# Optimization experiments

Hardware: AMD Instinct MI355X
Metric: run time of the kernel (lower is better)

## Reference

```python
import jax, jax.numpy as jnp
import numpy as np
import math

N_HEADS = 16

def setup_inputs() -> dict:
    key = jax.random.key(0)
    ks = jax.random.split(key, 5)
    B, S, D = 4, 2048, 1024
    scale = 0.02
    return {
        "x": jax.random.normal(ks[0], (B, S, D), dtype=jnp.float32),
        "w_in": jax.random.normal(ks[1], (D, 3 * D), dtype=jnp.float32) * scale,
        "b_in": jax.random.normal(ks[2], (3 * D,), dtype=jnp.float32) * scale,
        "w_out": jax.random.normal(ks[3], (D, D), dtype=jnp.float32) * scale,
        "b_out": jax.random.normal(ks[4], (D,), dtype=jnp.float32) * scale,
    }

def reference(x, w_in, b_in, w_out, b_out):
    B, S, D = x.shape
    H = N_HEADS
    dh = D // H
    qkv = x @ w_in + b_in                      # [B,S,3D]
    q, k, v = jnp.split(qkv, 3, axis=-1)
    # [B,S,D] -> [B,H,S,dh]
    q = q.reshape(B, S, H, dh).transpose(0, 2, 1, 3)
    k = k.reshape(B, S, H, dh).transpose(0, 2, 1, 3)
    v = v.reshape(B, S, H, dh).transpose(0, 2, 1, 3)
    scores = jnp.einsum("bhqd,bhkd->bhqk", q, k) / math.sqrt(dh)
    causal = jnp.tril(jnp.ones((S, S), dtype=bool))  # allow k <= q
    scores = jnp.where(causal, scores, -jnp.inf)
    wei = jax.nn.softmax(scores, axis=-1)
    out = jnp.einsum("bhqk,bhkd->bhqd", wei, v)      # [B,H,S,dh]
    out = out.transpose(0, 2, 1, 3).reshape(B, S, D)
    return out @ w_out + b_out
```

## Files before the change

kernel.cpp:

```cpp
#include <hip/hip_runtime.h>

typedef unsigned short u16;
typedef unsigned int   u32;
typedef float  f32x4  __attribute__((ext_vector_type(4)));
typedef __bf16 bf16x8 __attribute__((ext_vector_type(8)));
typedef __bf16 bf16x4 __attribute__((ext_vector_type(4)));
typedef short  s16x4  __attribute__((ext_vector_type(4)));
typedef unsigned short u16x8 __attribute__((ext_vector_type(8)));
typedef unsigned int   u32x4 __attribute__((ext_vector_type(4)));

__device__ __forceinline__ u16 f2bf(float f) {
  u32 u = __builtin_bit_cast(u32, f);
  u = (u + 0x7fffu + ((u >> 16) & 1u)) >> 16;
  return (u16)u;
}

__device__ __forceinline__ void gload_lds16(const void* g, void* l) {
  __builtin_amdgcn_global_load_lds(
      (const __attribute__((address_space(1))) void*)g,
      (__attribute__((address_space(3))) void*)l, 16, 0, 0);
}

__global__ __launch_bounds__(256) void conv_f32_bf16(
    const float* __restrict__ in, u16* __restrict__ out, int n8) {
  int i = blockIdx.x * 256 + threadIdx.x;
  if (i >= n8) return;
  const float4* p = (const float4*)in;
  float4 a = p[2 * i], b = p[2 * i + 1];
  u16x8 r;
  r[0] = f2bf(a.x); r[1] = f2bf(a.y); r[2] = f2bf(a.z); r[3] = f2bf(a.w);
  r[4] = f2bf(b.x); r[5] = f2bf(b.y); r[6] = f2bf(b.z); r[7] = f2bf(b.w);
  ((u16x8*)out)[i] = r;
}

__global__ __launch_bounds__(256) void conv_transpose(
    const float* __restrict__ in, u16* __restrict__ out, int K, int N) {
  __shared__ float tile[64][65];
  int nb = N >> 6;
  int tk = blockIdx.x / nb, tn = blockIdx.x % nb;
  int t = threadIdx.x;
  int kl = t >> 4, n4 = (t & 15) * 4;
#pragma unroll
  for (int i = 0; i < 4; ++i) {
    int k = kl + 16 * i;
    float4 v = *(const float4*)(in + (size_t)(tk * 64 + k) * N + tn * 64 + n4);
    tile[k][n4] = v.x; tile[k][n4 + 1] = v.y; tile[k][n4 + 2] = v.z; tile[k][n4 + 3] = v.w;
  }
  __syncthreads();
  int nl = t >> 4, k4 = (t & 15) * 4;
#pragma unroll
  for (int i = 0; i < 4; ++i) {
    int n = nl + 16 * i;
    ushort4 o;
    o.x = f2bf(tile[k4 + 0][n]); o.y = f2bf(tile[k4 + 1][n]);
    o.z = f2bf(tile[k4 + 2][n]); o.w = f2bf(tile[k4 + 3][n]);
    *(ushort4*)(out + (size_t)(tn * 64 + n) * K + tk * 64 + k4) = o;
  }
}

template <int OUT_BF16>
__global__ __launch_bounds__(256, 2) void gemm_kernel(
    const u16* __restrict__ A, const u16* __restrict__ Bt,
    const float* __restrict__ bias, void* __restrict__ C,
    int M, int N, int K) {
  __shared__ __align__(16) char smem[32768];
  char* As = smem;
  char* Bs = smem + 16384;
  int tid = threadIdx.x, w = tid >> 6, lane = tid & 63;
  int g = lane >> 4, l15 = lane & 15, l7 = lane & 7;
  int nblk = N >> 7;
  int bm = blockIdx.x / nblk, bn = blockIdx.x % nblk;
  int m0 = bm << 7, n0 = bn << 7;
  int wm = w >> 1, wn = w & 1;

  f32x4 acc[4][4];
#pragma unroll
  for (int i = 0; i < 4; ++i)
#pragma unroll
    for (int j = 0; j < 4; ++j) acc[i][j] = f32x4{0.f, 0.f, 0.f, 0.f};

  int kiter = K >> 6;
  for (int kt = 0; kt < kiter; ++kt) {
    __syncthreads();
#pragma unroll
    for (int i = 0; i < 4; ++i) {
      int rbase = 32 * w + 8 * i;
      int row = rbase + (lane >> 3);
      int koff = kt * 64 + 8 * (l7 ^ (row & 7));
      gload_lds16(A + (size_t)(m0 + row) * K + koff, As + rbase * 128);
      gload_lds16(Bt + (size_t)(n0 + row) * K + koff, Bs + rbase * 128);
    }
    __syncthreads();
#pragma unroll
    for (int ks = 0; ks < 2; ++ks) {
      bf16x8 af[4], bf[4];
#pragma unroll
      for (int mi = 0; mi < 4; ++mi) {
        int ml = wm * 64 + mi * 16 + l15;
        af[mi] = *(const bf16x8*)(As + ml * 128 + ((ks * 64 + g * 16) ^ ((ml & 7) << 4)));
      }
#pragma unroll
      for (int ni = 0; ni < 4; ++ni) {
        int nl = wn * 64 + ni * 16 + l15;
        bf[ni] = *(const bf16x8*)(Bs + nl * 128 + ((ks * 64 + g * 16) ^ ((nl & 7) << 4)));
      }
#pragma unroll
      for (int mi = 0; mi < 4; ++mi)
#pragma unroll
        for (int ni = 0; ni < 4; ++ni)
          acc[mi][ni] = __builtin_amdgcn_mfma_f32_16x16x32_bf16(af[mi], bf[ni], acc[mi][ni], 0, 0, 0);
    }
  }

#pragma unroll
  for (int ni = 0; ni < 4; ++ni) {
    int col = n0 + wn * 64 + ni * 16 + l15;
    float bv = bias[col];
#pragma unroll
    for (int mi = 0; mi < 4; ++mi) {
      int rowb = m0 + wm * 64 + mi * 16 + g * 4;
#pragma unroll
      for (int r = 0; r < 4; ++r) {
        float v = acc[mi][ni][r] + bv;
        if (OUT_BF16)
          ((u16*)C)[(size_t)(rowb + r) * N + col] = f2bf(v);
        else
          ((float*)C)[(size_t)(rowb + r) * N + col] = v;
      }
    }
  }
}


#if __has_builtin(__builtin_amdgcn_mfma_f32_16x16x16bf16_1k)
#define HAVE_MFMA16 1
__device__ __forceinline__ f32x4 mfma16(s16x4 a, s16x4 b, f32x4 c) {
  return __builtin_amdgcn_mfma_f32_16x16x16bf16_1k(a, b, c, 0, 0, 0);
}
#endif

struct V2reg { u16x8 a, b; };

__device__ __forceinline__ void stage_k(const u16* qb, char* kbuf, int kvt,
                                        int h, int w, int lane) {
  int l7 = lane & 7;
#pragma unroll
  for (int i = 0; i < 2; ++i) {
    int rbase = w * 16 + i * 8;
    int row = rbase + (lane >> 3);
    const u16* src = qb + (size_t)(kvt * 64 + row) * 3072 + 1024 + h * 64 + 8 * (l7 ^ (row & 7));
    gload_lds16(src, kbuf + rbase * 128);
  }
}

__device__ __forceinline__ V2reg load_v(const u16* qb, int kvt, int h, int kv0, int d0) {
  const u16* vs = qb + (size_t)(kvt * 64 + kv0) * 3072 + 2048 + h * 64 + d0;
  V2reg r;
  r.a = *(const u16x8*)vs;
  r.b = *(const u16x8*)(vs + 3072);
  return r;
}

__device__ __forceinline__ void write_v(char* vbuf, V2reg v, int kv0, int d0) {
#pragma unroll
  for (int j = 0; j < 8; ++j) {
    int d = d0 + j;
    u32 val = (u32)v.a[j] | ((u32)v.b[j] << 16);
    int sw = ((d & 7) ^ (d >> 3)) << 4;
    *(u32*)(vbuf + d * 128 + ((2 * kv0) ^ sw)) = val;
  }
}

__global__ __launch_bounds__(256, 2) void attn_fwd(
    const u16* __restrict__ qkv, u16* __restrict__ aout) {
  const int S = 2048, D3 = 3072;
  int bh = blockIdx.x & 63;
  int qt = 31 - (blockIdx.x >> 6);
  int b = bh >> 4, h = bh & 15;
  const u16* qb = qkv + (size_t)b * S * D3;

  int tid = threadIdx.x;
  int w = tid >> 6, lane = tid & 63;
  int g = lane >> 4, l15 = lane & 15, l7 = lane & 7;

  __shared__ __align__(16) char Kb[2][8192];
  __shared__ __align__(16) char Vb[2][8192];

  int qrow = qt * 64 + w * 16 + l15;
  const u16* qp = qb + (size_t)qrow * D3 + h * 64 + g * 8;
  bf16x8 qf0 = *(const bf16x8*)qp;
  bf16x8 qf1 = *(const bf16x8*)(qp + 32);

  f32x4 oaT[4];
#pragma unroll
  for (int i = 0; i < 4; ++i) oaT[i] = f32x4{0.f, 0.f, 0.f, 0.f};
  float m_s = -3e38f, l_s = 0.f;

  int vkv0 = w * 16 + ((lane >> 3) << 1);
  int vd0 = l7 * 8;

  stage_k(qb, Kb[0], 0, h, w, lane);
  {
    V2reg v = load_v(qb, 0, h, vkv0, vd0);
    write_v(Vb[0], v, vkv0, vd0);
  }
  __syncthreads();

  V2reg vreg;
  for (int kvt = 0; kvt <= qt; ++kvt) {
    int cur = kvt & 1;
    if (kvt < qt) {
      stage_k(qb, Kb[cur ^ 1], kvt + 1, h, w, lane);
      vreg = load_v(qb, kvt + 1, h, vkv0, vd0);
    }

    f32x4 sT[4];
    __builtin_amdgcn_s_setprio(1);
#pragma unroll
    for (int nb = 0; nb < 4; ++nb) {
      int kv = nb * 16 + l15;
      const char* kb = Kb[cur] + kv * 128;
      int sw = (kv & 7) << 4;
      bf16x8 kf0 = *(const bf16x8*)(kb + ((g * 16) ^ sw));
      bf16x8 kf1 = *(const bf16x8*)(kb + ((64 + g * 16) ^ sw));
      f32x4 z = {0.f, 0.f, 0.f, 0.f};
      z = __builtin_amdgcn_mfma_f32_16x16x32_bf16(kf0, qf0, z, 0, 0, 0);
      z = __builtin_amdgcn_mfma_f32_16x16x32_bf16(kf1, qf1, z, 0, 0, 0);
      sT[nb] = z;
    }
    __builtin_amdgcn_s_setprio(0);

#pragma unroll
    for (int nb = 0; nb < 4; ++nb)
#pragma unroll
      for (int r = 0; r < 4; ++r) sT[nb][r] *= 0.125f;
    if (kvt == qt) {
      int qloc = w * 16 + l15;
#pragma unroll
      for (int nb = 0; nb < 4; ++nb)
#pragma unroll
        for (int r = 0; r < 4; ++r)
          if (nb * 16 + g * 4 + r > qloc) sT[nb][r] = -1e30f;
    }

    float pm = -3e38f;
#pragma unroll
    for (int nb = 0; nb < 4; ++nb)
#pragma unroll
      for (int r = 0; r < 4; ++r) pm = fmaxf(pm, sT[nb][r]);
    pm = fmaxf(pm, __shfl_xor(pm, 16));
    pm = fmaxf(pm, __shfl_xor(pm, 32));
    float newm = fmaxf(m_s, pm);
    float corr = __expf(m_s - newm);
    float rs = 0.f;
#pragma unroll
    for (int nb = 0; nb < 4; ++nb)
#pragma unroll
      for (int r = 0; r < 4; ++r) {
        float e = __expf(sT[nb][r] - newm);
        sT[nb][r] = e;
        rs += e;
      }
    rs += __shfl_xor(rs, 16);
    rs += __shfl_xor(rs, 32);
    l_s = l_s * corr + rs;
    m_s = newm;
#pragma unroll
    for (int db = 0; db < 4; ++db)
#pragma unroll
      for (int r = 0; r < 4; ++r) oaT[db][r] *= corr;

#ifdef HAVE_MFMA16
    s16x4 pf[4];
#pragma unroll
    for (int nb = 0; nb < 4; ++nb) {
      bf16x4 t;
#pragma unroll
      for (int r = 0; r < 4; ++r) t[r] = (__bf16)sT[nb][r];
      pf[nb] = __builtin_bit_cast(s16x4, t);
    }
    __builtin_amdgcn_s_setprio(1);
#pragma unroll
    for (int db = 0; db < 4; ++db) {
      int d = db * 16 + l15;
      const char* vb = Vb[cur] + d * 128;
      int swd = ((d & 7) ^ (d >> 3)) << 4;
#pragma unroll
      for (int nb = 0; nb < 4; ++nb) {
        bf16x4 vf = *(const bf16x4*)(vb + ((nb * 32 + g * 8) ^ swd));
        oaT[db] = mfma16(__builtin_bit_cast(s16x4, vf), pf[nb], oaT[db]);
      }
    }
    __builtin_amdgcn_s_setprio(0);
#else
    u32 wlo[4], whi[4];
#pragma unroll
    for (int nb = 0; nb < 4; ++nb) {
      wlo[nb] = (u32)f2bf(sT[nb][0]) | ((u32)f2bf(sT[nb][1]) << 16);
      whi[nb] = (u32)f2bf(sT[nb][2]) | ((u32)f2bf(sT[nb][3]) << 16);
    }
    int srcA = (2 * (g & 1)) * 16 + l15;
    int srcB = srcA + 16;
    bool hi = (g >> 1) != 0;
    __builtin_amdgcn_s_setprio(1);
#pragma unroll
    for (int kb2 = 0; kb2 < 2; ++kb2) {
      int nbE = kb2 * 2, nbO = kb2 * 2 + 1;
      u32 a0 = __shfl(wlo[nbE], srcA), a1 = __shfl(whi[nbE], srcA);
      u32 a2 = __shfl(wlo[nbE], srcB), a3 = __shfl(whi[nbE], srcB);
      u32 b0 = __shfl(wlo[nbO], srcA), b1 = __shfl(whi[nbO], srcA);
      u32 b2 = __shfl(wlo[nbO], srcB), b3 = __shfl(whi[nbO], srcB);
      u32x4 ow = {hi ? b0 : a0, hi ? b1 : a1, hi ? b2 : a2, hi ? b3 : a3};
      bf16x8 pfrag = __builtin_bit_cast(bf16x8, ow);
#pragma unroll
      for (int db = 0; db < 4; ++db) {
        int d = db * 16 + l15;
        int swd = ((d & 7) ^ (d >> 3)) << 4;
        bf16x8 vf = *(const bf16x8*)(Vb[cur] + d * 128 + ((kb2 * 64 + g * 16) ^ swd));
        oaT[db] = __builtin_amdgcn_mfma_f32_16x16x32_bf16(vf, pfrag, oaT[db], 0, 0, 0);
      }
    }
    __builtin_amdgcn_s_setprio(0);
#endif

    if (kvt < qt) {
      write_v(Vb[cur ^ 1], vreg, vkv0, vd0);
      __syncthreads();
    }
  }

  float inv = 1.0f / l_s;
  size_t obase = (size_t)(b * S + qt * 64 + w * 16 + l15) * 1024 + h * 64;
#pragma unroll
  for (int db = 0; db < 4; ++db) {
    ushort4 st;
    st.x = f2bf(oaT[db][0] * inv);
    st.y = f2bf(oaT[db][1] * inv);
    st.z = f2bf(oaT[db][2] * inv);
    st.w = f2bf(oaT[db][3] * inv);
    *(ushort4*)(aout + obase + db * 16 + g * 4) = st;
  }
}

extern "C" void kernel_launch(void* const* d_in, const int* in_sizes, int n_in,
                              void* d_out, int out_size, void* d_ws, size_t ws_size,
                              hipStream_t stream) {
  (void)in_sizes; (void)n_in; (void)out_size;
  const float* x     = (const float*)d_in[0];
  const float* w_in  = (const float*)d_in[1];
  const float* b_in  = (const float*)d_in[2];
  const float* w_out = (const float*)d_in[3];
  const float* b_out = (const float*)d_in[4];
  float* out = (float*)d_out;
  char* ws = (char*)d_ws;
  if (ws_size < 92274688u) return;

  u16* xb     = (u16*)(ws);
  u16* w_inT  = (u16*)(ws + (16u << 20));
  u16* w_outT = (u16*)(ws + (22u << 20));
  u16* qkv    = (u16*)(ws + (24u << 20));
  u16* aout   = (u16*)(ws + (72u << 20));

  conv_f32_bf16<<<4096, 256, 0, stream>>>(x, xb, 1048576);
  conv_transpose<<<768, 256, 0, stream>>>(w_in, w_inT, 1024, 3072);
  conv_transpose<<<256, 256, 0, stream>>>(w_out, w_outT, 1024, 1024);
  gemm_kernel<1><<<1536, 256, 0, stream>>>(xb, w_inT, b_in, qkv, 8192, 3072, 1024);
  attn_fwd<<<2048, 256, 0, stream>>>(qkv, aout);
  gemm_kernel<0><<<512, 256, 0, stream>>>(aout, w_outT, b_out, out, 8192, 1024, 1024);
}
```

Baseline: 261.9 us.

## Fold softmax scale into QKV GEMM, lazy rescale, MFMA row sums, XCD block remap

The QKV GEMM epilogue now multiplies Q columns by 0.125*log2(e), so attention can drop its per-score scaling and use exp2 directly. The online softmax rescales the running max only when some lane's max grows by more than 8, which skips most correction multiplies. Row sums are accumulated by an MFMA against a vector of ones instead of shuffle reductions. The GEMMs also remap block ids across the 8 XCDs, and the attention launch bound is raised to 4 blocks per CU. Costs are an extra MFMA per tile, an extra bf16 rounding of the scaled Q values, a small overflow margin from the lazy max, and tighter register limits that could cause spills.

```diff
diff --git a/kernel.cpp b/kernel.cpp
--- a/kernel.cpp
+++ b/kernel.cpp
@@ -58,7 +58,7 @@
   }
 }
 
-template <int OUT_BF16>
+template <int OUT_BF16, int SCALE_Q>
 __global__ __launch_bounds__(256, 2) void gemm_kernel(
     const u16* __restrict__ A, const u16* __restrict__ Bt,
     const float* __restrict__ bias, void* __restrict__ C,
@@ -68,8 +68,10 @@
   char* Bs = smem + 16384;
   int tid = threadIdx.x, w = tid >> 6, lane = tid & 63;
   int g = lane >> 4, l15 = lane & 15, l7 = lane & 7;
+  int cpx = (int)gridDim.x >> 3;
+  int bid = (blockIdx.x & 7) * cpx + (blockIdx.x >> 3);
   int nblk = N >> 7;
-  int bm = blockIdx.x / nblk, bn = blockIdx.x % nblk;
+  int bm = bid / nblk, bn = bid % nblk;
   int m0 = bm << 7, n0 = bn << 7;
   int wm = w >> 1, wn = w & 1;
 
@@ -116,12 +118,13 @@
   for (int ni = 0; ni < 4; ++ni) {
     int col = n0 + wn * 64 + ni * 16 + l15;
     float bv = bias[col];
+    float sc = (SCALE_Q && col < 1024) ? 0.18033688011112042f : 1.0f;
 #pragma unroll
     for (int mi = 0; mi < 4; ++mi) {
       int rowb = m0 + wm * 64 + mi * 16 + g * 4;
 #pragma unroll
       for (int r = 0; r < 4; ++r) {
-        float v = acc[mi][ni][r] + bv;
+        float v = (acc[mi][ni][r] + bv) * sc;
         if (OUT_BF16)
           ((u16*)C)[(size_t)(rowb + r) * N + col] = f2bf(v);
         else
@@ -171,7 +174,7 @@
   }
 }
 
-__global__ __launch_bounds__(256, 2) void attn_fwd(
+__global__ __launch_bounds__(256, 4) void attn_fwd(
     const u16* __restrict__ qkv, u16* __restrict__ aout) {
   const int S = 2048, D3 = 3072;
   int bh = blockIdx.x & 63;
@@ -194,7 +197,8 @@
   f32x4 oaT[4];
 #pragma unroll
   for (int i = 0; i < 4; ++i) oaT[i] = f32x4{0.f, 0.f, 0.f, 0.f};
-  float m_s = -3e38f, l_s = 0.f;
+  f32x4 l_acc = {0.f, 0.f, 0.f, 0.f};
+  float m_s = -3e38f;
 
   int vkv0 = w * 16 + ((lane >> 3) << 1);
   int vd0 = l7 * 8;
@@ -230,10 +234,6 @@
     }
     __builtin_amdgcn_s_setprio(0);
 
-#pragma unroll
-    for (int nb = 0; nb < 4; ++nb)
-#pragma unroll
-      for (int r = 0; r < 4; ++r) sT[nb][r] *= 0.125f;
     if (kvt == qt) {
       int qloc = w * 16 + l15;
 #pragma unroll
@@ -250,25 +250,21 @@
       for (int r = 0; r < 4; ++r) pm = fmaxf(pm, sT[nb][r]);
     pm = fmaxf(pm, __shfl_xor(pm, 16));
     pm = fmaxf(pm, __shfl_xor(pm, 32));
-    float newm = fmaxf(m_s, pm);
-    float corr = __expf(m_s - newm);
-    float rs = 0.f;
+    if (!__all(pm - m_s <= 8.0f)) {
+      float newm = fmaxf(m_s, pm);
+      float corr = __builtin_amdgcn_exp2f(m_s - newm);
+      m_s = newm;
+      l_acc[0] *= corr;
+#pragma unroll
+      for (int db = 0; db < 4; ++db)
+#pragma unroll
+        for (int r = 0; r < 4; ++r) oaT[db][r] *= corr;
+    }
 #pragma unroll
     for (int nb = 0; nb < 4; ++nb)
 #pragma unroll
-      for (int r = 0; r < 4; ++r) {
-        float e = __expf(sT[nb][r] - newm);
-        sT[nb][r] = e;
-        rs += e;
-      }
-    rs += __shfl_xor(rs, 16);
-    rs += __shfl_xor(rs, 32);
-    l_s = l_s * corr + rs;
-    m_s = newm;
-#pragma unroll
-    for (int db = 0; db < 4; ++db)
-#pragma unroll
-      for (int r = 0; r < 4; ++r) oaT[db][r] *= corr;
+      for (int r = 0; r < 4; ++r)
+        sT[nb][r] = __builtin_amdgcn_exp2f(sT[nb][r] - m_s);
 
 #ifdef HAVE_MFMA16
     s16x4 pf[4];
@@ -279,7 +275,12 @@
       for (int r = 0; r < 4; ++r) t[r] = (__bf16)sT[nb][r];
       pf[nb] = __builtin_bit_cast(s16x4, t);
     }
+    s16x4 ones;
+#pragma unroll
+    for (int r = 0; r < 4; ++r) ones[r] = (short)0x3F80;
     __builtin_amdgcn_s_setprio(1);
+#pragma unroll
+    for (int nb = 0; nb < 4; ++nb) l_acc = mfma16(ones, pf[nb], l_acc);
 #pragma unroll
     for (int db = 0; db < 4; ++db) {
       int d = db * 16 + l15;
@@ -302,6 +303,9 @@
     int srcA = (2 * (g & 1)) * 16 + l15;
     int srcB = srcA + 16;
     bool hi = (g >> 1) != 0;
+    bf16x8 ones8;
+#pragma unroll
+    for (int j = 0; j < 8; ++j) ones8[j] = __builtin_bit_cast(__bf16, (u16)0x3F80);
     __builtin_amdgcn_s_setprio(1);
 #pragma unroll
     for (int kb2 = 0; kb2 < 2; ++kb2) {
@@ -312,6 +316,7 @@
       u32 b2 = __shfl(wlo[nbO], srcB), b3 = __shfl(whi[nbO], srcB);
       u32x4 ow = {hi ? b0 : a0, hi ? b1 : a1, hi ? b2 : a2, hi ? b3 : a3};
       bf16x8 pfrag = __builtin_bit_cast(bf16x8, ow);
+      l_acc = __builtin_amdgcn_mfma_f32_16x16x32_bf16(ones8, pfrag, l_acc, 0, 0, 0);
 #pragma unroll
       for (int db = 0; db < 4; ++db) {
         int d = db * 16 + l15;
@@ -329,7 +334,7 @@
     }
   }
 
-  float inv = 1.0f / l_s;
+  float inv = 1.0f / l_acc[0];
   size_t obase = (size_t)(b * S + qt * 64 + w * 16 + l15) * 1024 + h * 64;
 #pragma unroll
   for (int db = 0; db < 4; ++db) {
@@ -364,7 +369,7 @@
   conv_f32_bf16<<<4096, 256, 0, stream>>>(x, xb, 1048576);
   conv_transpose<<<768, 256, 0, stream>>>(w_in, w_inT, 1024, 3072);
   conv_transpose<<<256, 256, 0, stream>>>(w_out, w_outT, 1024, 1024);
-  gemm_kernel<1><<<1536, 256, 0, stream>>>(xb, w_inT, b_in, qkv, 8192, 3072, 1024);
+  gemm_kernel<1, 1><<<1536, 256, 0, stream>>>(xb, w_inT, b_in, qkv, 8192, 3072, 1024);
   attn_fwd<<<2048, 256, 0, stream>>>(qkv, aout);
-  gemm_kernel<0><<<512, 256, 0, stream>>>(aout, w_outT, b_out, out, 8192, 1024, 1024);
-}
+  gemm_kernel<0, 0><<<512, 256, 0, stream>>>(aout, w_outT, b_out, out, 8192, 1024, 1024);
+}
```

Result: no change. 259.2 us (-1.0%).
